# Performance work log

Measured on AMD Instinct MI355X. Metric: run time of the kernel, lower is better.

Reference implementation:

```python
import jax, jax.numpy as jnp
import numpy as np

N_NODES = 100000


def gcn_conv(x, edge_index, W, num_nodes):
    """PyG GCNConv (bias=False): add self-loops, symmetric normalization,
    out[c] = sum_{(r,c) in E'} deg^{-1/2}[r] * deg^{-1/2}[c] * (x @ W)[r]."""
    h = x @ W  # [N, out_dim]
    row, col = edge_index[0], edge_index[1]
    loop = jnp.arange(num_nodes, dtype=row.dtype)
    row = jnp.concatenate([row, loop])
    col = jnp.concatenate([col, loop])
    ones = jnp.ones(row.shape[0], dtype=h.dtype)
    deg = jax.ops.segment_sum(ones, col, num_segments=num_nodes)  # [N]
    dinv = jnp.where(deg > 0, jax.lax.rsqrt(deg), 0.0)
    norm = dinv[row] * dinv[col]  # [E+N]
    msgs = norm[:, None] * h[row]  # gather + scale
    return jax.ops.segment_sum(msgs, col, num_segments=num_nodes)  # scatter-add


def setup_inputs() -> dict:
    key = jax.random.key(0)
    k1, k2, k3, k4 = jax.random.split(key, 4)
    x = jax.random.normal(k1, (N_NODES, 128), dtype=jnp.float32)
    edge_index = jax.random.randint(k2, (2, 3200000), 0, N_NODES, dtype=jnp.int64)
    W1 = jax.random.normal(k3, (128, 32), dtype=jnp.float32) * (1.0 / np.sqrt(128))
    W2 = jax.random.normal(k4, (32, 3), dtype=jnp.float32) * (1.0 / np.sqrt(32))
    return {"x": x, "edge_index": edge_index, "W1": W1, "W2": W2}


def reference(x, edge_index, W1, W2):
    n = x.shape[0]
    hidden1 = jnp.tanh(gcn_conv(x, edge_index, W1, n))  # dropout p=0.0 -> identity
    z = gcn_conv(hidden1, edge_index, W2, n)
    return z  # original returns (z, z, None)
```

## Files before the change

kernel.cpp:

```cpp
#include <hip/hip_runtime.h>
#include <hip/hip_fp16.h>

#define N_NODES 100000
#define N_EDGES 3200000
#define F_IN    128
#define F_HID   32

#define BSHIFT  7
#define BKSZ    128
#define NBKT    ((N_NODES + BKSZ - 1) / BKSZ)
#define CAP     5120
#define CHUNK   4096
#define NBLK_E  ((N_EDGES + CHUNK - 1) / CHUNK)
#define RBITS   17
#define RMASK   0x1FFFF

typedef _Float16 f16;
typedef f16   f16x8 __attribute__((ext_vector_type(8)));
typedef float f32x4 __attribute__((ext_vector_type(4)));
#define WPAD 136

__device__ __forceinline__ float fast_tanh(float x) {
    float t = __builtin_amdgcn_exp2f(x * 2.88539008f);
    return 1.0f - 2.0f * __builtin_amdgcn_rcpf(t + 1.0f);
}


__global__ __launch_bounds__(512) void k_part(const int* __restrict__ row, const int* __restrict__ col,
                                              int* __restrict__ gcur, unsigned* __restrict__ bkt) {
    __shared__ int hist[NBKT];
    __shared__ int lbase[NBKT];
    __shared__ int gbase[NBKT];
    __shared__ unsigned perm[CHUNK];
    __shared__ unsigned short pb[CHUNK];
    __shared__ int wt[8];
    int t = threadIdx.x;
    for (int i = t; i < NBKT; i += 512) hist[i] = 0;
    __syncthreads();

    int e0 = blockIdx.x * CHUNK;
    int n  = min(CHUNK, N_EDGES - e0);
    int r[8], c[8], rk[8];
#pragma unroll
    for (int k = 0; k < 8; k++) {
        int idx = t + k * 512;
        if (idx < n) {
            r[k]  = row[e0 + idx];
            c[k]  = col[e0 + idx];
            rk[k] = atomicAdd(&hist[c[k] >> BSHIFT], 1);
        }
    }
    __syncthreads();

    {
        int b0 = t * 2;
        int s0 = (b0     < NBKT) ? hist[b0]     : 0;
        int s1 = (b0 + 1 < NBKT) ? hist[b0 + 1] : 0;
        int tsum = s0 + s1;
        int lane = t & 63, wid = t >> 6;
        int incl = tsum;
#pragma unroll
        for (int sh = 1; sh < 64; sh <<= 1) {
            int u = __shfl_up(incl, sh);
            if (lane >= sh) incl += u;
        }
        if (lane == 63) wt[wid] = incl;
        __syncthreads();
        int wpre = 0;
        for (int w = 0; w < wid; w++) wpre += wt[w];
        int excl = wpre + incl - tsum;
        if (b0     < NBKT) lbase[b0]     = excl;
        if (b0 + 1 < NBKT) lbase[b0 + 1] = excl + s0;
    }
    for (int i = t; i < NBKT; i += 512) {
        int h = hist[i];
        gbase[i] = i * CAP + (h ? atomicAdd(&gcur[i], h) : 0);
    }
    __syncthreads();

#pragma unroll
    for (int k = 0; k < 8; k++) {
        int idx = t + k * 512;
        if (idx < n) {
            int b   = c[k] >> BSHIFT;
            int pos = lbase[b] + rk[k];
            perm[pos] = (unsigned)r[k] | ((unsigned)(c[k] & (BKSZ - 1)) << RBITS);
            pb[pos]   = (unsigned short)b;
        }
    }
    __syncthreads();

    for (int i = t; i < n; i += 512) {
        int b = pb[i];
        bkt[gbase[b] + (i - lbase[b])] = perm[i];
    }
}


__global__ __launch_bounds__(1024) void k_bucket(unsigned* __restrict__ bkt,
                                                 const int* __restrict__ gcur,
                                                 int* __restrict__ off, int* __restrict__ end,
                                                 float* __restrict__ dinv) {
    __shared__ unsigned stg[CAP];
    __shared__ int cnt[BKSZ];
    __shared__ int cur[BKSZ];
    __shared__ int wtot[2];
    int t = threadIdx.x, b = blockIdx.x;
    int s = b * CAP, m = gcur[b];
    if (t < BKSZ) cnt[t] = 0;
    __syncthreads();
    for (int i = t; i < m; i += 1024) {
        unsigned x = bkt[s + i];
        stg[i] = x;
        atomicAdd(&cnt[x >> RBITS], 1);
    }
    __syncthreads();

    int lane = t & 63, wid = t >> 6;
    int v = 0, v4 = 0, incl = 0;
    if (t < BKSZ) {
        v  = cnt[t];
        v4 = (v + 3) & ~3;
        incl = v4;
        #pragma unroll
        for (int sh = 1; sh < 64; sh <<= 1) {
            int u = __shfl_up(incl, sh);
            if (lane >= sh) incl += u;
        }
        if (lane == 63) wtot[wid] = incl;
    }
    __syncthreads();
    if (t < BKSZ) {
        int wpre = (wid == 1) ? wtot[0] : 0;
        int excl = wpre + incl - v4;
        int base = s + excl;
        cur[t] = base;
        int g = b * BKSZ + t;
        if (g < N_NODES) {
            off[g]  = base;
            end[g]  = base + v4;
            dinv[g] = rsqrtf((float)(v + 1));
        }
        for (int j = v; j < v4; j++) bkt[base + j] = N_NODES;
    }
    __syncthreads();
    for (int i = t; i < m; i += 1024) {
        unsigned x = stg[i];
        int p = atomicAdd(&cur[x >> RBITS], 1);
        bkt[p] = x & RMASK;
    }
}


__global__ __launch_bounds__(256) void k_gemm1(const float* __restrict__ x, const float* __restrict__ W1,
                                               const float* __restrict__ dinv, unsigned* __restrict__ h1s) {
    __shared__ f16 WH[F_HID * WPAD];
    __shared__ f16 XH[4][16 * WPAD];
    int t = threadIdx.x;
    for (int i = t; i < F_IN * F_HID; i += 256) {
        int k = i >> 5, f = i & 31;
        WH[f * WPAD + k] = (f16)W1[i];
    }
    if (blockIdx.x == 0 && t < 8)
        ((uint2*)h1s)[(size_t)N_NODES * 8 + t] = make_uint2(0u, 0u);
    __syncthreads();

    int l = t & 63, w = t >> 6;
    int tile = blockIdx.x * 4 + w;
    if (tile >= N_NODES / 16) return;
    int R0 = tile * 16;

    {
        int row = l >> 2, seg = l & 3;
        const float4* xg = (const float4*)(x + (size_t)(R0 + row) * F_IN) + seg * 8;
        f16* dst = &XH[w][row * WPAD + seg * 32];
#pragma unroll
        for (int j = 0; j < 4; j++) {
            float4 a = xg[2 * j], b = xg[2 * j + 1];
            f16x8 v;
            v[0] = (f16)a.x; v[1] = (f16)a.y; v[2] = (f16)a.z; v[3] = (f16)a.w;
            v[4] = (f16)b.x; v[5] = (f16)b.y; v[6] = (f16)b.z; v[7] = (f16)b.w;
            *(f16x8*)(dst + j * 8) = v;
        }
    }

    f32x4 acc0 = {0.f, 0.f, 0.f, 0.f};
    f32x4 acc1 = {0.f, 0.f, 0.f, 0.f};
    int lo = l & 15, hi = l >> 4;
    const f16* arow  = &XH[w][lo * WPAD + hi * 8];
    const f16* b0row = &WH[lo * WPAD + hi * 8];
    const f16* b1row = &WH[(16 + lo) * WPAD + hi * 8];
#pragma unroll
    for (int s = 0; s < 4; s++) {
        f16x8 af  = *(const f16x8*)(arow  + s * 32);
        f16x8 bf0 = *(const f16x8*)(b0row + s * 32);
        f16x8 bf1 = *(const f16x8*)(b1row + s * 32);
        acc0 = __builtin_amdgcn_mfma_f32_16x16x32_f16(af, bf0, acc0, 0, 0, 0);
        acc1 = __builtin_amdgcn_mfma_f32_16x16x32_f16(af, bf1, acc1, 0, 0, 0);
    }

    _Float16* h1h = (_Float16*)h1s;
    int rbase = R0 + hi * 4;
#pragma unroll
    for (int i = 0; i < 4; i++) {
        float d = dinv[rbase + i];
        h1h[(size_t)(rbase + i) * 32 + lo]      = (f16)(d * acc0[i]);
        h1h[(size_t)(rbase + i) * 32 + 16 + lo] = (f16)(d * acc1[i]);
    }
}


__global__ __launch_bounds__(256) void k_conv1(const int* __restrict__ off, const int* __restrict__ end,
                                               const int* __restrict__ srt, const float* __restrict__ dinv,
                                               const unsigned* __restrict__ h1s,
                                               const float* __restrict__ W2, float* __restrict__ h2s4) {
    int t = threadIdx.x;
    if (blockIdx.x == 0 && t < 4) h2s4[(size_t)N_NODES * 4 + t] = 0.0f;
    int lane = t & 63, wid = t >> 6;
    int q = lane >> 3, o = lane & 7;
    int c = (blockIdx.x * 4 + wid) * 8 + q;

    int b = off[c], ep = end[c];
    const char* h1b = (const char*)h1s;
    unsigned oo = (unsigned)(o << 3);
    uint2 sv = *(const uint2*)(h1b + (((unsigned)c << 6) + oo));

    float a0a = 0.f, a1a = 0.f, a2a = 0.f, a3a = 0.f;
    float a0b = 0.f, a1b = 0.f, a2b = 0.f, a3b = 0.f;
    float a0c = 0.f, a1c = 0.f, a2c = 0.f, a3c = 0.f;
    float a0d = 0.f, a1d = 0.f, a2d = 0.f, a3d = 0.f;

    int p = b;
    while (__any(p < ep)) {
        int r0 = N_NODES, r1 = N_NODES, r2 = N_NODES, r3 = N_NODES;
        if (p < ep) {
            int4 rs = *(const int4*)(srt + p);
            r0 = rs.x; r1 = rs.y; r2 = rs.z; r3 = rs.w;
        }
        uint2 v0 = *(const uint2*)(h1b + (((unsigned)r0 << 6) + oo));
        uint2 v1 = *(const uint2*)(h1b + (((unsigned)r1 << 6) + oo));
        uint2 v2 = *(const uint2*)(h1b + (((unsigned)r2 << 6) + oo));
        uint2 v3 = *(const uint2*)(h1b + (((unsigned)r3 << 6) + oo));
        a0a += __low2float(*(const __half2*)&v0.x);  a1a += __high2float(*(const __half2*)&v0.x);
        a2a += __low2float(*(const __half2*)&v0.y);  a3a += __high2float(*(const __half2*)&v0.y);
        a0b += __low2float(*(const __half2*)&v1.x);  a1b += __high2float(*(const __half2*)&v1.x);
        a2b += __low2float(*(const __half2*)&v1.y);  a3b += __high2float(*(const __half2*)&v1.y);
        a0c += __low2float(*(const __half2*)&v2.x);  a1c += __high2float(*(const __half2*)&v2.x);
        a2c += __low2float(*(const __half2*)&v2.y);  a3c += __high2float(*(const __half2*)&v2.y);
        a0d += __low2float(*(const __half2*)&v3.x);  a1d += __high2float(*(const __half2*)&v3.x);
        a2d += __low2float(*(const __half2*)&v3.y);  a3d += __high2float(*(const __half2*)&v3.y);
        p += 4;
    }

    float di = dinv[c];
    float f0 = (a0a + a0b) + (a0c + a0d) + __low2float(*(const __half2*)&sv.x);
    float f1 = (a1a + a1b) + (a1c + a1d) + __high2float(*(const __half2*)&sv.x);
    float f2 = (a2a + a2b) + (a2c + a2d) + __low2float(*(const __half2*)&sv.y);
    float f3 = (a3a + a3b) + (a3c + a3d) + __high2float(*(const __half2*)&sv.y);

    float h0 = fast_tanh(di * f0);
    float h1 = fast_tanh(di * f1);
    float h2 = fast_tanh(di * f2);
    float h3 = fast_tanh(di * f3);

    const float* Wp = W2 + (o << 2) * 3;
    float p0 = h0 * Wp[0] + h1 * Wp[3] + h2 * Wp[6] + h3 * Wp[9];
    float p1 = h0 * Wp[1] + h1 * Wp[4] + h2 * Wp[7] + h3 * Wp[10];
    float p2 = h0 * Wp[2] + h1 * Wp[5] + h2 * Wp[8] + h3 * Wp[11];
#pragma unroll
    for (int m = 1; m <= 4; m <<= 1) {
        p0 += __shfl_xor(p0, m);
        p1 += __shfl_xor(p1, m);
        p2 += __shfl_xor(p2, m);
    }
    if (o < 4) {
        float vv = (o == 0) ? p0 : (o == 1) ? p1 : (o == 2) ? p2 : 0.0f;
        h2s4[(size_t)c * 4 + o] = (o < 3) ? di * vv : 0.0f;
    }
}


__global__ __launch_bounds__(256) void k_conv2(const int* __restrict__ off, const int* __restrict__ end,
                                               const int* __restrict__ srt, const float* __restrict__ dinv,
                                               const float* __restrict__ h2s4, float* __restrict__ out) {
    int gt = blockIdx.x * 256 + threadIdx.x;
    int c = gt >> 2, j = gt & 3;
    if (c >= N_NODES) return;

    const float4* h2v = (const float4*)h2s4;
    int b = off[c], ep = end[c];
    float4 sv = h2v[c];
    float ax = (j == 0) ? sv.x : 0.0f;
    float ay = (j == 0) ? sv.y : 0.0f;
    float az = (j == 0) ? sv.z : 0.0f;

    for (int p = b + 4 * j; p < ep; p += 16) {
        int4 rs = *(const int4*)(srt + p);
        float4 v0 = h2v[rs.x];
        float4 v1 = h2v[rs.y];
        float4 v2 = h2v[rs.z];
        float4 v3 = h2v[rs.w];
        ax += (v0.x + v1.x) + (v2.x + v3.x);
        ay += (v0.y + v1.y) + (v2.y + v3.y);
        az += (v0.z + v1.z) + (v2.z + v3.z);
    }
#pragma unroll
    for (int m = 1; m <= 2; m <<= 1) {
        ax += __shfl_xor(ax, m);
        ay += __shfl_xor(ay, m);
        az += __shfl_xor(az, m);
    }

    float di = dinv[c];
    if (j < 3) {
        float a = (j == 0) ? ax : (j == 1) ? ay : az;
        out[(size_t)c * 3 + j] = di * a;
    }
}


extern "C" void kernel_launch(void* const* d_in, const int* in_sizes, int n_in,
                              void* d_out, int out_size, void* d_ws, size_t ws_size,
                              hipStream_t stream) {
    const float* x   = (const float*)d_in[0];
    const int*   ei  = (const int*)d_in[1];
    const float* W1  = (const float*)d_in[2];
    const float* W2  = (const float*)d_in[3];
    float*       out = (float*)d_out;

    const int* row = ei;
    const int* col = ei + N_EDGES;

    char* ws = (char*)d_ws;
    unsigned* bkt = (unsigned*)ws;
    int*      srt = (int*)ws;
    char*     p   = ws + 4ull * NBKT * CAP;
    int*      gcur = (int*)p;                 p += 4ull * ((NBKT + 63) & ~63);
    int*      off  = (int*)p;                 p += 4ull * N_NODES;
    int*      end  = (int*)p;                 p += 4ull * N_NODES;
    float*    dinv = (float*)p;               p += 4ull * N_NODES;
    unsigned* h1s  = (unsigned*)p;            p += 64ull * (N_NODES + 1);
    float*    h2s4 = (float*)p;

    const int B = 256;
    const int NTILE = N_NODES / 16;
    hipMemsetAsync(gcur, 0, 4ull * NBKT, stream);
    hipLaunchKernelGGL(k_part,   dim3(NBLK_E), dim3(512),  0, stream, row, col, gcur, bkt);
    hipLaunchKernelGGL(k_bucket, dim3(NBKT),   dim3(1024), 0, stream, bkt, gcur, off, end, dinv);
    hipLaunchKernelGGL(k_gemm1,  dim3((NTILE + 3) / 4), dim3(B), 0, stream, x, W1, dinv, h1s);
    hipLaunchKernelGGL(k_conv1,  dim3(N_NODES / 32), dim3(B), 0, stream,
                       off, end, srt, dinv, h1s, W2, h2s4);
    hipLaunchKernelGGL(k_conv2,  dim3((4 * N_NODES + B - 1) / B), dim3(B), 0, stream,
                       off, end, srt, dinv, h2s4, out);
}
```

Before: 215.4 us.

## Fuse first-layer GEMM into bucket kernel using idle warps

Removes the separate k_gemm1 launch and computes x@W1 scaled by dinv inside k_bucket. Half the threads do the CSR scatter and the other 8 warps each compute a 16-row MFMA tile for the block's 128 nodes, using dinv values already held in shared memory. The goal is to save a kernel launch and a global dinv round-trip and to overlap the GEMM with the scatter. In exchange the scatter loop now uses 512 threads instead of 1024, and the block uses more LDS for W1 and the x tiles, which may lower occupancy.

```diff
diff --git a/kernel.cpp b/kernel.cpp
--- a/kernel.cpp
+++ b/kernel.cpp
@@ -100,19 +100,30 @@
 __global__ __launch_bounds__(1024) void k_bucket(unsigned* __restrict__ bkt,
                                                  const int* __restrict__ gcur,
                                                  int* __restrict__ off, int* __restrict__ end,
-                                                 float* __restrict__ dinv) {
+                                                 float* __restrict__ dinv,
+                                                 const float* __restrict__ x,
+                                                 const float* __restrict__ W1,
+                                                 unsigned* __restrict__ h1s) {
     __shared__ unsigned stg[CAP];
     __shared__ int cnt[BKSZ];
-    __shared__ int cur[BKSZ];
     __shared__ int wtot[2];
+    __shared__ float dlds[BKSZ];
+    __shared__ f16 WH[F_HID * WPAD];
+    __shared__ f16 XH[8][16 * WPAD];
     int t = threadIdx.x, b = blockIdx.x;
     int s = b * CAP, m = gcur[b];
     if (t < BKSZ) cnt[t] = 0;
+    for (int i = t; i < F_IN * F_HID; i += 1024) {
+        int k = i >> 5, f = i & 31;
+        WH[f * WPAD + k] = (f16)W1[i];
+    }
+    if (b == 0 && t < 8)
+        ((uint2*)h1s)[(size_t)N_NODES * 8 + t] = make_uint2(0u, 0u);
     __syncthreads();
     for (int i = t; i < m; i += 1024) {
-        unsigned x = bkt[s + i];
-        stg[i] = x;
-        atomicAdd(&cnt[x >> RBITS], 1);
+        unsigned xx = bkt[s + i];
+        stg[i] = xx;
+        atomicAdd(&cnt[xx >> RBITS], 1);
     }
     __syncthreads();
 
@@ -134,78 +145,67 @@
         int wpre = (wid == 1) ? wtot[0] : 0;
         int excl = wpre + incl - v4;
         int base = s + excl;
-        cur[t] = base;
+        cnt[t] = base;
         int g = b * BKSZ + t;
+        float dv = rsqrtf((float)(v + 1));
+        dlds[t] = dv;
         if (g < N_NODES) {
             off[g]  = base;
             end[g]  = base + v4;
-            dinv[g] = rsqrtf((float)(v + 1));
+            dinv[g] = dv;
         }
         for (int j = v; j < v4; j++) bkt[base + j] = N_NODES;
     }
     __syncthreads();
-    for (int i = t; i < m; i += 1024) {
-        unsigned x = stg[i];
-        int p = atomicAdd(&cur[x >> RBITS], 1);
-        bkt[p] = x & RMASK;
-    }
-}
-
-
-__global__ __launch_bounds__(256) void k_gemm1(const float* __restrict__ x, const float* __restrict__ W1,
-                                               const float* __restrict__ dinv, unsigned* __restrict__ h1s) {
-    __shared__ f16 WH[F_HID * WPAD];
-    __shared__ f16 XH[4][16 * WPAD];
-    int t = threadIdx.x;
-    for (int i = t; i < F_IN * F_HID; i += 256) {
-        int k = i >> 5, f = i & 31;
-        WH[f * WPAD + k] = (f16)W1[i];
-    }
-    if (blockIdx.x == 0 && t < 8)
-        ((uint2*)h1s)[(size_t)N_NODES * 8 + t] = make_uint2(0u, 0u);
-    __syncthreads();
-
-    int l = t & 63, w = t >> 6;
-    int tile = blockIdx.x * 4 + w;
-    if (tile >= N_NODES / 16) return;
-    int R0 = tile * 16;
-
-    {
-        int row = l >> 2, seg = l & 3;
-        const float4* xg = (const float4*)(x + (size_t)(R0 + row) * F_IN) + seg * 8;
-        f16* dst = &XH[w][row * WPAD + seg * 32];
-#pragma unroll
-        for (int j = 0; j < 4; j++) {
-            float4 a = xg[2 * j], b = xg[2 * j + 1];
-            f16x8 v;
-            v[0] = (f16)a.x; v[1] = (f16)a.y; v[2] = (f16)a.z; v[3] = (f16)a.w;
-            v[4] = (f16)b.x; v[5] = (f16)b.y; v[6] = (f16)b.z; v[7] = (f16)b.w;
-            *(f16x8*)(dst + j * 8) = v;
-        }
-    }
-
-    f32x4 acc0 = {0.f, 0.f, 0.f, 0.f};
-    f32x4 acc1 = {0.f, 0.f, 0.f, 0.f};
-    int lo = l & 15, hi = l >> 4;
-    const f16* arow  = &XH[w][lo * WPAD + hi * 8];
-    const f16* b0row = &WH[lo * WPAD + hi * 8];
-    const f16* b1row = &WH[(16 + lo) * WPAD + hi * 8];
-#pragma unroll
-    for (int s = 0; s < 4; s++) {
-        f16x8 af  = *(const f16x8*)(arow  + s * 32);
-        f16x8 bf0 = *(const f16x8*)(b0row + s * 32);
-        f16x8 bf1 = *(const f16x8*)(b1row + s * 32);
-        acc0 = __builtin_amdgcn_mfma_f32_16x16x32_f16(af, bf0, acc0, 0, 0, 0);
-        acc1 = __builtin_amdgcn_mfma_f32_16x16x32_f16(af, bf1, acc1, 0, 0, 0);
-    }
-
-    _Float16* h1h = (_Float16*)h1s;
-    int rbase = R0 + hi * 4;
-#pragma unroll
-    for (int i = 0; i < 4; i++) {
-        float d = dinv[rbase + i];
-        h1h[(size_t)(rbase + i) * 32 + lo]      = (f16)(d * acc0[i]);
-        h1h[(size_t)(rbase + i) * 32 + 16 + lo] = (f16)(d * acc1[i]);
+
+    if (t < 512) {
+        for (int i = t; i < m; i += 512) {
+            unsigned xx = stg[i];
+            int p = atomicAdd(&cnt[xx >> RBITS], 1);
+            bkt[p] = xx & RMASK;
+        }
+    } else {
+        int w = (t >> 6) - 8;
+        int l = t & 63;
+        int R0 = b * BKSZ + w * 16;
+        if (R0 < N_NODES) {
+            int row = l >> 2, seg = l & 3;
+            const float4* xg = (const float4*)(x + (size_t)(R0 + row) * F_IN) + seg * 8;
+            f16* dst = &XH[w][row * WPAD + seg * 32];
+#pragma unroll
+            for (int j = 0; j < 4; j++) {
+                float4 a = xg[2 * j], bb = xg[2 * j + 1];
+                f16x8 vv;
+                vv[0] = (f16)a.x;  vv[1] = (f16)a.y;  vv[2] = (f16)a.z;  vv[3] = (f16)a.w;
+                vv[4] = (f16)bb.x; vv[5] = (f16)bb.y; vv[6] = (f16)bb.z; vv[7] = (f16)bb.w;
+                *(f16x8*)(dst + j * 8) = vv;
+            }
+
+            f32x4 acc0 = {0.f, 0.f, 0.f, 0.f};
+            f32x4 acc1 = {0.f, 0.f, 0.f, 0.f};
+            int lo = l & 15, hi = l >> 4;
+            const f16* arow  = &XH[w][lo * WPAD + hi * 8];
+            const f16* b0row = &WH[lo * WPAD + hi * 8];
+            const f16* b1row = &WH[(16 + lo) * WPAD + hi * 8];
+#pragma unroll
+            for (int ss = 0; ss < 4; ss++) {
+                f16x8 af  = *(const f16x8*)(arow  + ss * 32);
+                f16x8 bf0 = *(const f16x8*)(b0row + ss * 32);
+                f16x8 bf1 = *(const f16x8*)(b1row + ss * 32);
+                acc0 = __builtin_amdgcn_mfma_f32_16x16x32_f16(af, bf0, acc0, 0, 0, 0);
+                acc1 = __builtin_amdgcn_mfma_f32_16x16x32_f16(af, bf1, acc1, 0, 0, 0);
+            }
+
+            _Float16* h1h = (_Float16*)h1s;
+            int rbase = R0 + hi * 4;
+            int lbase_ = w * 16 + hi * 4;
+#pragma unroll
+            for (int i = 0; i < 4; i++) {
+                float d = dlds[lbase_ + i];
+                h1h[(size_t)(rbase + i) * 32 + lo]      = (f16)(d * acc0[i]);
+                h1h[(size_t)(rbase + i) * 32 + 16 + lo] = (f16)(d * acc1[i]);
+            }
+        }
     }
 }
 
@@ -343,11 +343,10 @@
     float*    h2s4 = (float*)p;
 
     const int B = 256;
-    const int NTILE = N_NODES / 16;
     hipMemsetAsync(gcur, 0, 4ull * NBKT, stream);
     hipLaunchKernelGGL(k_part,   dim3(NBLK_E), dim3(512),  0, stream, row, col, gcur, bkt);
-    hipLaunchKernelGGL(k_bucket, dim3(NBKT),   dim3(1024), 0, stream, bkt, gcur, off, end, dinv);
-    hipLaunchKernelGGL(k_gemm1,  dim3((NTILE + 3) / 4), dim3(B), 0, stream, x, W1, dinv, h1s);
+    hipLaunchKernelGGL(k_bucket, dim3(NBKT),   dim3(1024), 0, stream,
+                       bkt, gcur, off, end, dinv, x, W1, h1s);
     hipLaunchKernelGGL(k_conv1,  dim3(N_NODES / 32), dim3(B), 0, stream,
                        off, end, srt, dinv, h1s, W2, h2s4);
     hipLaunchKernelGGL(k_conv2,  dim3((4 * N_NODES + B - 1) / B), dim3(B), 0, stream,
```

After: 211.4 us (median of 2 runs). Within noise of the previous version (-1.8%).
